# Kernel tuning notes

Measured on AMD Instinct MI355X. Metric: run time of the kernel, lower is better.

The kernel has to match this reference:

```python
import jax, jax.numpy as jnp
import numpy as np

HEADS = 16
DIM_HEAD = 64
DIM = 1024
LN_EPS = 1e-5


def _split_heads(x):
    # [b, n, h*d] -> [b, h, n, d]
    b, n, _ = x.shape
    return x.reshape(b, n, HEADS, DIM_HEAD).transpose(0, 2, 1, 3)


def _rmsnorm(x, gamma):
    # F.normalize over last dim, then * sqrt(dim_head) * gamma ([h,1,d])
    nrm = jnp.sqrt(jnp.sum(x * x, axis=-1, keepdims=True))
    normed = x / jnp.maximum(nrm, 1e-12)
    return normed * (DIM_HEAD ** 0.5) * gamma


def setup_inputs() -> dict:
    key = jax.random.key(0)
    ks = jax.random.split(key, 8)
    inner = HEADS * DIM_HEAD
    q = jax.random.normal(ks[0], (8, 128, DIM), dtype=jnp.float32)
    kv = jax.random.normal(ks[1], (8, 4096, DIM), dtype=jnp.float32)
    mask = jax.random.bernoulli(ks[2], 0.9, (8, 4096))  # bool, True = keep
    ln_w = jnp.ones((DIM,), dtype=jnp.float32)
    gamma_q = jnp.ones((HEADS, 1, DIM_HEAD), dtype=jnp.float32)
    gamma_k = jnp.ones((HEADS, 1, DIM_HEAD), dtype=jnp.float32)
    s = 1.0 / np.sqrt(DIM)
    Wq = jax.random.normal(ks[3], (DIM, inner), dtype=jnp.float32) * s
    Wkv = jax.random.normal(ks[4], (DIM, 2 * inner), dtype=jnp.float32) * s
    Wout = jax.random.normal(ks[5], (inner, DIM), dtype=jnp.float32) * (1.0 / np.sqrt(inner))
    return {"q": q, "kv": kv, "mask": mask, "ln_w": ln_w,
            "gamma_q": gamma_q, "gamma_k": gamma_k,
            "Wq": Wq, "Wkv": Wkv, "Wout": Wout}


def reference(q, kv, mask, ln_w, gamma_q, gamma_k, Wq, Wkv, Wout):
    # LayerNorm (no bias) on queries only
    mu = jnp.mean(q, axis=-1, keepdims=True)
    var = jnp.mean(jnp.square(q - mu), axis=-1, keepdims=True)
    qn = (q - mu) / jnp.sqrt(var + LN_EPS) * ln_w

    inner = HEADS * DIM_HEAD
    Q = qn @ Wq                      # [b, nq, inner]
    KVp = kv @ Wkv                   # [b, nkv, 2*inner]
    K, V = KVp[..., :inner], KVp[..., inner:]

    Qh = _rmsnorm(_split_heads(Q), gamma_q)   # [b, h, nq, d]
    Kh = _rmsnorm(_split_heads(K), gamma_k)   # [b, h, nkv, d]
    Vh = _split_heads(V)                      # [b, h, nkv, d]

    dots = jnp.einsum('bhnd,bhmd->bhnm', Qh, Kh)  # no 1/sqrt(d): scale lives in RMSNorm
    neg = -jnp.finfo(dots.dtype).max
    dots = jnp.where(mask[:, None, None, :], dots, neg)
    attn = jax.nn.softmax(dots, axis=-1)

    out = jnp.einsum('bhnm,bhmd->bhnd', attn, Vh)
    b, h, n, d = out.shape
    out = out.transpose(0, 2, 1, 3).reshape(b, n, h * d)
    return out @ Wout
```

## Files before the change

### kernel.cpp

```cpp
#include <hip/hip_runtime.h>
#include <cfloat>
#include <cstdint>


typedef _Float16 f16;
typedef _Float16 f16x8 __attribute__((ext_vector_type(8)));
typedef _Float16 f16x4 __attribute__((ext_vector_type(4)));
typedef float    f32x4 __attribute__((ext_vector_type(4)));

#define DEV __device__ __forceinline__

DEV f32x4 mfma16(f16x8 a, f16x8 b, f32x4 c) {
  return __builtin_amdgcn_mfma_f32_16x16x32_f16(a, b, c, 0, 0, 0);
}

DEV void gl_lds16(const void* g, void* l) {
  __builtin_amdgcn_global_load_lds(
      (const __attribute__((address_space(1))) uint32_t*)g,
      (__attribute__((address_space(3))) uint32_t*)l, 16, 0, 0);
}


__global__ __launch_bounds__(256) void cast_f16_kernel(
    const float* __restrict__ src, f16* __restrict__ dst, int n4) {
  int stride = gridDim.x * 256;
  for (int i = blockIdx.x * 256 + threadIdx.x; i < n4; i += stride) {
    float4 v = ((const float4*)src)[i];
    f16x4 o = { (f16)v.x, (f16)v.y, (f16)v.z, (f16)v.w };
    ((f16x4*)dst)[i] = o;
  }
}

__global__ __launch_bounds__(256) void transpose_cast_kernel(
    const float* __restrict__ src, f16* __restrict__ dst, int ldsrc, int lddst) {
  __shared__ float tile[32][33];
  int c0 = blockIdx.x * 32, r0 = blockIdx.y * 32;
  int tx = threadIdx.x & 31, ty = threadIdx.x >> 5;
  #pragma unroll
  for (int i = 0; i < 4; ++i)
    tile[ty + i * 8][tx] = src[(long)(r0 + ty + i * 8) * ldsrc + c0 + tx];
  __syncthreads();
  #pragma unroll
  for (int i = 0; i < 4; ++i)
    dst[(long)(c0 + ty + i * 8) * lddst + r0 + tx] = (f16)tile[tx][ty + i * 8];
}

__global__ __launch_bounds__(256) void ln_kernel(
    const float* __restrict__ q, const float* __restrict__ w, f16* __restrict__ qn) {
  int row = blockIdx.x, tid = threadIdx.x;
  float4 v = ((const float4*)(q + (long)row * 1024))[tid];
  float s1 = v.x + v.y + v.z + v.w;
  float s2 = v.x * v.x + v.y * v.y + v.z * v.z + v.w * v.w;
  #pragma unroll
  for (int off = 1; off < 64; off <<= 1) {
    s1 += __shfl_xor(s1, off);
    s2 += __shfl_xor(s2, off);
  }
  __shared__ float r1[4], r2[4];
  int wid = tid >> 6;
  if ((tid & 63) == 0) { r1[wid] = s1; r2[wid] = s2; }
  __syncthreads();
  s1 = r1[0] + r1[1] + r1[2] + r1[3];
  s2 = r2[0] + r2[1] + r2[2] + r2[3];
  float mu = s1 * (1.0f / 1024.0f);
  float var = s2 * (1.0f / 1024.0f) - mu * mu;
  float rstd = rsqrtf(var + 1e-5f);
  float4 wv = ((const float4*)w)[tid];
  f16x4 o = { (f16)((v.x - mu) * rstd * wv.x), (f16)((v.y - mu) * rstd * wv.y),
              (f16)((v.z - mu) * rstd * wv.z), (f16)((v.w - mu) * rstd * wv.w) };
  ((f16x4*)(qn + (long)row * 1024))[tid] = o;
}

template <int OUT_F16, int NORM>
__global__ __launch_bounds__(256) void gemm128(
    const f16* __restrict__ A, const f16* __restrict__ BT, void* __restrict__ C,
    const float* __restrict__ gamma,
    int M, int N, int K, int lda, int ldb, int ldc) {
  __shared__ f16 tA[128 * 32];
  __shared__ f16 tB[128 * 32];
  const int tid = threadIdx.x, lane = tid & 63, wid = tid >> 6;
  const int wr = wid >> 1, wc = wid & 1;
  const int c = lane & 15, g = lane >> 4;
  const int m0 = blockIdx.y * 128, n0 = blockIdx.x * 128;
  f32x4 acc[4][4] = {};
  for (int k0 = 0; k0 < K; k0 += 32) {
    __syncthreads();
    #pragma unroll
    for (int ii = 0; ii < 2; ++ii) {
      int i = tid + ii * 256;
      gl_lds16(A + (long)(m0 + (i >> 2)) * lda + k0 + (i & 3) * 8, tA + i * 8);
    }
    #pragma unroll
    for (int ii = 0; ii < 2; ++ii) {
      int i = tid + ii * 256;
      gl_lds16(BT + (long)(n0 + (i >> 2)) * ldb + k0 + (i & 3) * 8, tB + i * 8);
    }
    __syncthreads();
    f16x8 af[4], bfr[4];
    #pragma unroll
    for (int mi = 0; mi < 4; ++mi)
      af[mi] = *(const f16x8*)&tA[(wr * 64 + mi * 16 + c) * 32 + g * 8];
    #pragma unroll
    for (int ni = 0; ni < 4; ++ni)
      bfr[ni] = *(const f16x8*)&tB[(wc * 64 + ni * 16 + c) * 32 + g * 8];
    #pragma unroll
    for (int mi = 0; mi < 4; ++mi)
      #pragma unroll
      for (int ni = 0; ni < 4; ++ni)
        acc[mi][ni] = mfma16(af[mi], bfr[ni], acc[mi][ni]);
  }
  float gam[4];
  if (NORM) {
    #pragma unroll
    for (int ni = 0; ni < 4; ++ni) gam[ni] = gamma[n0 + wc * 64 + ni * 16 + c];
    #pragma unroll
    for (int mi = 0; mi < 4; ++mi)
      #pragma unroll
      for (int j = 0; j < 4; ++j) {
        float s = 0.f;
        #pragma unroll
        for (int ni = 0; ni < 4; ++ni) { float x = acc[mi][ni][j]; s += x * x; }
        s += __shfl_xor(s, 1); s += __shfl_xor(s, 2);
        s += __shfl_xor(s, 4); s += __shfl_xor(s, 8);
        float sc = 8.0f / fmaxf(sqrtf(s), 1e-12f);
        #pragma unroll
        for (int ni = 0; ni < 4; ++ni) acc[mi][ni][j] *= sc * gam[ni];
      }
  }
  #pragma unroll
  for (int mi = 0; mi < 4; ++mi)
    #pragma unroll
    for (int ni = 0; ni < 4; ++ni)
      #pragma unroll
      for (int j = 0; j < 4; ++j) {
        int row = m0 + wr * 64 + mi * 16 + g * 4 + j;
        int col = n0 + wc * 64 + ni * 16 + c;
        if (OUT_F16) ((f16*)C)[(long)row * ldc + col] = (f16)acc[mi][ni][j];
        else        ((float*)C)[(long)row * ldc + col] = acc[mi][ni][j];
      }
}

__global__ __launch_bounds__(512, 2) void gemm256(
    const f16* __restrict__ A, const f16* __restrict__ BT, f16* __restrict__ C,
    const float* __restrict__ gamma, int normLim,
    int K, int lda, int ldb, int ldc, int mtiles, int ntiles) {
  __shared__ f16 lds[4 * 16384];
  const int tid = threadIdx.x, lane = tid & 63, wid = tid >> 6;
  const int wr = wid >> 2, wc = wid & 3;
  const int c = lane & 15, g = lane >> 4;
  const int nwg = mtiles * ntiles, cpx = nwg >> 3;
  const int bid = blockIdx.x;
  const int wg = (bid & 7) * cpx + (bid >> 3);
  const int n0 = (wg % ntiles) * 256;
  const long m0 = (long)(wg / ntiles) * 256;

  const int nkt = K >> 5;
  const int r1 = tid >> 2, r2 = 128 + (tid >> 2), sl = tid & 3;
  const int sw1 = (sl ^ ((r1 >> 1) & 3)) << 3, sw2 = (sl ^ ((r2 >> 1) & 3)) << 3;

  f32x4 acc[8][4] = {};

  #define STAGE_A(kt_) do { int kt__ = (kt_);                                   \
    f16* dst = lds + ((kt__) & 3) * 16384; int k0 = (kt__) << 5;                \
    gl_lds16(A + (m0 + r1) * lda + k0 + sw1, dst + (long)tid * 8);              \
    gl_lds16(A + (m0 + r2) * lda + k0 + sw2, dst + (long)(tid + 512) * 8);      \
  } while (0)
  #define STAGE_B(kt_) do { int kt__ = (kt_);                                   \
    f16* dst = lds + ((kt__) & 3) * 16384 + 8192; int k0 = (kt__) << 5;         \
    gl_lds16(BT + (long)(n0 + r1) * ldb + k0 + sw1, dst + (long)tid * 8);       \
    gl_lds16(BT + (long)(n0 + r2) * ldb + k0 + sw2, dst + (long)(tid + 512) * 8);\
  } while (0)

  STAGE_A(0); STAGE_B(0); STAGE_A(1); STAGE_B(1);
  asm volatile("s_waitcnt vmcnt(4)" ::: "memory");
  __builtin_amdgcn_s_barrier();

  for (int kt = 0; kt < nkt; ++kt) {
    const f16* la = lds + (kt & 3) * 16384;
    const f16* lb = la + 8192;
    const bool pre = (kt + 2) < nkt;
    if (pre) STAGE_A(kt + 2);
    f16x8 bfr[4], afr[4];
    #pragma unroll
    for (int ni = 0; ni < 4; ++ni) {
      int r = wc * 64 + ni * 16 + c;
      bfr[ni] = *(const f16x8*)&lb[r * 32 + ((g ^ ((r >> 1) & 3)) << 3)];
    }
    #pragma unroll
    for (int q = 0; q < 4; ++q) {
      int r = wr * 128 + q * 16 + c;
      afr[q] = *(const f16x8*)&la[r * 32 + ((g ^ ((r >> 1) & 3)) << 3)];
    }
    __builtin_amdgcn_s_setprio(1);
    #pragma unroll
    for (int q = 0; q < 4; ++q)
      #pragma unroll
      for (int ni = 0; ni < 4; ++ni)
        acc[q][ni] = mfma16(afr[q], bfr[ni], acc[q][ni]);
    __builtin_amdgcn_s_setprio(0);
    if (pre) STAGE_B(kt + 2);
    #pragma unroll
    for (int q = 0; q < 4; ++q) {
      int r = wr * 128 + 64 + q * 16 + c;
      afr[q] = *(const f16x8*)&la[r * 32 + ((g ^ ((r >> 1) & 3)) << 3)];
    }
    __builtin_amdgcn_s_setprio(1);
    #pragma unroll
    for (int q = 0; q < 4; ++q)
      #pragma unroll
      for (int ni = 0; ni < 4; ++ni)
        acc[4 + q][ni] = mfma16(afr[q], bfr[ni], acc[4 + q][ni]);
    __builtin_amdgcn_s_setprio(0);
    if (pre) { asm volatile("s_waitcnt vmcnt(4)" ::: "memory"); }
    else     { asm volatile("s_waitcnt vmcnt(0)" ::: "memory"); }
    __builtin_amdgcn_s_barrier();
  }
  #undef STAGE_A
  #undef STAGE_B

  const int colbase = n0 + wc * 64;
  if (colbase < normLim) {
    float gam[4];
    #pragma unroll
    for (int ni = 0; ni < 4; ++ni) gam[ni] = gamma[colbase + ni * 16 + c];
    #pragma unroll
    for (int mi = 0; mi < 8; ++mi)
      #pragma unroll
      for (int j = 0; j < 4; ++j) {
        float s = 0.f;
        #pragma unroll
        for (int ni = 0; ni < 4; ++ni) { float x = acc[mi][ni][j]; s += x * x; }
        s += __shfl_xor(s, 1); s += __shfl_xor(s, 2);
        s += __shfl_xor(s, 4); s += __shfl_xor(s, 8);
        float sc = 8.0f / fmaxf(sqrtf(s), 1e-12f);
        #pragma unroll
        for (int ni = 0; ni < 4; ++ni) acc[mi][ni][j] *= sc * gam[ni];
      }
  }
  #pragma unroll
  for (int mi = 0; mi < 8; ++mi)
    #pragma unroll
    for (int j = 0; j < 4; ++j) {
      long row = m0 + wr * 128 + mi * 16 + g * 4 + j;
      #pragma unroll
      for (int ni = 0; ni < 4; ++ni)
        C[row * ldc + colbase + ni * 16 + c] = (f16)acc[mi][ni][j];
    }
}

__global__ __launch_bounds__(256) void attn_kernel(
    const f16* __restrict__ Q, const f16* __restrict__ KV,
    const int* __restrict__ mask, float* __restrict__ Opart,
    float* __restrict__ ml) {
  __shared__ f16 Kt[64 * 64];
  __shared__ f16 Vt[64 * 72];
  __shared__ f16 Pl[4 * 16 * 72];
  const int blk = blockIdx.x;
  const int chunk = blk >> 8, sub = blk & 255;
  const int half = sub & 1, h = (sub >> 1) & 15, b = sub >> 5;
  const int tid = threadIdx.x, lane = tid & 63, wid = tid >> 6;
  const int c = lane & 15, g = lane >> 4;

  const int qrow = b * 128 + half * 64 + wid * 16 + c;
  f16x8 qa[2];
  #pragma unroll
  for (int kk = 0; kk < 2; ++kk)
    qa[kk] = *(const f16x8*)&Q[(long)qrow * 1024 + h * 64 + kk * 32 + g * 8];

  float m_[4], l_[4];
  f32x4 o_[4];
  #pragma unroll
  for (int j = 0; j < 4; ++j) { m_[j] = -FLT_MAX; l_[j] = 0.f; }
  #pragma unroll
  for (int ni = 0; ni < 4; ++ni) o_[ni] = (f32x4){0.f, 0.f, 0.f, 0.f};

  const long kvbase = (long)b * 4096 * 2048;
  f16* Pw = Pl + wid * 16 * 72;

  for (int kt = chunk * 16; kt < chunk * 16 + 16; ++kt) {
    __syncthreads();
    #pragma unroll
    for (int ii = 0; ii < 2; ++ii) {
      int i = tid + ii * 256;
      int r = i >> 3, s = i & 7;
      gl_lds16(KV + kvbase + (long)(kt * 64 + r) * 2048 + h * 64 + ((s ^ (r & 7)) * 8),
               Kt + i * 8);
    }
    #pragma unroll
    for (int ii = 0; ii < 2; ++ii) {
      int i = tid + ii * 256;
      int kv = i & 63, d0 = (i >> 6) * 8;
      f16x8 v = *(const f16x8*)&KV[kvbase + (long)(kt * 64 + kv) * 2048 + 1024 + h * 64 + d0];
      #pragma unroll
      for (int j = 0; j < 8; ++j) Vt[(d0 + j) * 72 + kv] = v[j];
    }
    __syncthreads();

    f32x4 s4[4];
    #pragma unroll
    for (int ni = 0; ni < 4; ++ni) {
      s4[ni] = (f32x4){0.f, 0.f, 0.f, 0.f};
      int kvr = ni * 16 + c;
      #pragma unroll
      for (int kk = 0; kk < 2; ++kk) {
        int slot = (kk * 4 + g) ^ (kvr & 7);
        f16x8 kb = *(const f16x8*)&Kt[kvr * 64 + slot * 8];
        s4[ni] = mfma16(qa[kk], kb, s4[ni]);
      }
    }

    int msk[4];
    #pragma unroll
    for (int ni = 0; ni < 4; ++ni) {
      msk[ni] = mask[b * 4096 + kt * 64 + ni * 16 + c];
      if (!msk[ni]) s4[ni] = (f32x4){-FLT_MAX, -FLT_MAX, -FLT_MAX, -FLT_MAX};
    }

    float mnew[4], alpha[4], psum[4];
    #pragma unroll
    for (int j = 0; j < 4; ++j) {
      float v = fmaxf(fmaxf(s4[0][j], s4[1][j]), fmaxf(s4[2][j], s4[3][j]));
      v = fmaxf(v, __shfl_xor(v, 1));
      v = fmaxf(v, __shfl_xor(v, 2));
      v = fmaxf(v, __shfl_xor(v, 4));
      v = fmaxf(v, __shfl_xor(v, 8));
      mnew[j] = fmaxf(m_[j], v);
      alpha[j] = __expf(m_[j] - mnew[j]);
      m_[j] = mnew[j];
      psum[j] = 0.f;
    }
    f16 pb[4][4];
    #pragma unroll
    for (int ni = 0; ni < 4; ++ni)
      #pragma unroll
      for (int j = 0; j < 4; ++j) {
        float p = msk[ni] ? __expf(s4[ni][j] - mnew[j]) : 0.0f;
        psum[j] += p;
        pb[ni][j] = (f16)p;
      }
    #pragma unroll
    for (int j = 0; j < 4; ++j) {
      float ps = psum[j];
      ps += __shfl_xor(ps, 1);
      ps += __shfl_xor(ps, 2);
      ps += __shfl_xor(ps, 4);
      ps += __shfl_xor(ps, 8);
      l_[j] = alpha[j] * l_[j] + ps;
    }
    #pragma unroll
    for (int ni = 0; ni < 4; ++ni)
      #pragma unroll
      for (int j = 0; j < 4; ++j)
        Pw[(g * 4 + j) * 72 + ni * 16 + c] = pb[ni][j];
    #pragma unroll
    for (int ni = 0; ni < 4; ++ni)
      #pragma unroll
      for (int j = 0; j < 4; ++j)
        o_[ni][j] *= alpha[j];
    f16x8 pa[2];
    #pragma unroll
    for (int kk = 0; kk < 2; ++kk)
      pa[kk] = *(const f16x8*)&Pw[c * 72 + kk * 32 + g * 8];
    #pragma unroll
    for (int ni = 0; ni < 4; ++ni)
      #pragma unroll
      for (int kk = 0; kk < 2; ++kk) {
        f16x8 vb = *(const f16x8*)&Vt[(ni * 16 + c) * 72 + kk * 32 + g * 8];
        o_[ni] = mfma16(pa[kk], vb, o_[ni]);
      }
  }

  #pragma unroll
  for (int j = 0; j < 4; ++j) {
    int row = b * 128 + half * 64 + wid * 16 + g * 4 + j;
    #pragma unroll
    for (int ni = 0; ni < 4; ++ni)
      Opart[((long)chunk * 1024 + row) * 1024 + h * 64 + ni * 16 + c] = o_[ni][j];
    if (c == 0) {
      long u = (((long)chunk * 1024 + row) * 16 + h) * 2;
      ml[u] = m_[j];
      ml[u + 1] = l_[j];
    }
  }
}

__global__ __launch_bounds__(256) void attn_merge_kernel(
    const float* __restrict__ Opart, const float* __restrict__ ml,
    f16* __restrict__ Om) {
  int unit = blockIdx.x * 4 + (threadIdx.x >> 6);
  int lane = threadIdx.x & 63;
  int row = unit >> 4, h = unit & 15;
  float mc[4], lc[4], M = -FLT_MAX;
  #pragma unroll
  for (int cI = 0; cI < 4; ++cI) {
    long u = (((long)cI * 1024 + row) * 16 + h) * 2;
    mc[cI] = ml[u]; lc[cI] = ml[u + 1];
    M = fmaxf(M, mc[cI]);
  }
  float L = 0.f, o = 0.f;
  #pragma unroll
  for (int cI = 0; cI < 4; ++cI) {
    float w = __expf(mc[cI] - M);
    L += lc[cI] * w;
    o += Opart[((long)cI * 1024 + row) * 1024 + h * 64 + lane] * w;
  }
  Om[(long)row * 1024 + h * 64 + lane] = (f16)(o / fmaxf(L, 1e-30f));
}


extern "C" void kernel_launch(void* const* d_in, const int* in_sizes, int n_in,
                              void* d_out, int out_size, void* d_ws, size_t ws_size,
                              hipStream_t stream) {
  const float* q    = (const float*)d_in[0];
  const float* kv   = (const float*)d_in[1];
  const int*   mask = (const int*)d_in[2];
  const float* ln_w = (const float*)d_in[3];
  const float* gq   = (const float*)d_in[4];
  const float* gk   = (const float*)d_in[5];
  const float* Wq   = (const float*)d_in[6];
  const float* Wkv  = (const float*)d_in[7];
  const float* Wout = (const float*)d_in[8];
  float* out = (float*)d_out;
  char* ws = (char*)d_ws;
  const size_t MB = (size_t)1 << 20;
  f16* qn    = (f16*)(ws + 0 * MB);
  f16* Qm    = (f16*)(ws + 2 * MB);
  f16* Om    = (f16*)(ws + 4 * MB);
  f16* WqT   = (f16*)(ws + 6 * MB);
  f16* WkvT  = (f16*)(ws + 8 * MB);
  f16* WoutT = (f16*)(ws + 12 * MB);
  f16* kv16  = (f16*)(ws + 14 * MB);
  float* Opart = (float*)(ws + 14 * MB);
  float* mlb   = (float*)(ws + 30 * MB);
  f16* KVp   = (f16*)(ws + 78 * MB);

  cast_f16_kernel<<<2048, 256, 0, stream>>>(kv, kv16, 8 * 4096 * 1024 / 4);
  transpose_cast_kernel<<<dim3(32, 32), 256, 0, stream>>>(Wq, WqT, 1024, 1024);
  transpose_cast_kernel<<<dim3(64, 32), 256, 0, stream>>>(Wkv, WkvT, 2048, 1024);
  transpose_cast_kernel<<<dim3(32, 32), 256, 0, stream>>>(Wout, WoutT, 1024, 1024);
  ln_kernel<<<1024, 256, 0, stream>>>(q, ln_w, qn);
  gemm128<1, 1><<<dim3(8, 8), 256, 0, stream>>>(qn, WqT, Qm, gq,
                                                1024, 1024, 1024, 1024, 1024, 1024);
  gemm256<<<1024, 512, 0, stream>>>(kv16, WkvT, KVp, gk, 1024,
                                    1024, 1024, 1024, 2048, 128, 8);
  attn_kernel<<<1024, 256, 0, stream>>>(Qm, KVp, mask, Opart, mlb);
  attn_merge_kernel<<<4096, 256, 0, stream>>>(Opart, mlb, Om);
  gemm128<0, 0><<<dim3(8, 8), 256, 0, stream>>>(Om, WoutT, out, nullptr,
                                                1024, 1024, 1024, 1024, 1024, 1024);
}
```

Before: 515.5 us.

## Restructure KV GEMM into double-buffered 64-deep K pipeline and merge weight transposes

The 256x256 KV projection GEMM now stages 64-wide K slices into two LDS buffers. Its loop is unrolled into eight half-steps that interleave the next stage's global-to-LDS loads with MFMA blocks, and LDS fragment offsets are precomputed. The three weight transpose/cast launches are also merged into one kernel to cut launch overhead. The many extra barriers per iteration could add synchronization cost.

```diff
diff --git a/kernel.cpp b/kernel.cpp
--- a/kernel.cpp
+++ b/kernel.cpp
@@ -31,10 +31,19 @@
   }
 }
 
-__global__ __launch_bounds__(256) void transpose_cast_kernel(
-    const float* __restrict__ src, f16* __restrict__ dst, int ldsrc, int lddst) {
+__global__ __launch_bounds__(256) void transpose_all_kernel(
+    const float* __restrict__ Wq, const float* __restrict__ Wkv,
+    const float* __restrict__ Wout,
+    f16* __restrict__ WqT, f16* __restrict__ WkvT, f16* __restrict__ WoutT) {
   __shared__ float tile[32][33];
-  int c0 = blockIdx.x * 32, r0 = blockIdx.y * 32;
+  int b = blockIdx.x;
+  const float* src; f16* dst; int ldsrc, lddst, c0, r0;
+  if (b < 1024)      { src = Wq;   dst = WqT;   ldsrc = 1024; lddst = 1024;
+                       c0 = (b & 31) * 32;          r0 = (b >> 5) * 32; }
+  else if (b < 3072) { int bb = b - 1024; src = Wkv; dst = WkvT; ldsrc = 2048;
+                       lddst = 1024; c0 = (bb & 63) * 32; r0 = (bb >> 6) * 32; }
+  else               { int bb = b - 3072; src = Wout; dst = WoutT; ldsrc = 1024;
+                       lddst = 1024; c0 = (bb & 31) * 32; r0 = (bb >> 5) * 32; }
   int tx = threadIdx.x & 31, ty = threadIdx.x >> 5;
   #pragma unroll
   for (int i = 0; i < 4; ++i)
@@ -144,7 +153,7 @@
     const f16* __restrict__ A, const f16* __restrict__ BT, f16* __restrict__ C,
     const float* __restrict__ gamma, int normLim,
     int K, int lda, int ldb, int ldc, int mtiles, int ntiles) {
-  __shared__ f16 lds[4 * 16384];
+  __shared__ f16 lds[2 * 32768];
   const int tid = threadIdx.x, lane = tid & 63, wid = tid >> 6;
   const int wr = wid >> 2, wc = wid & 3;
   const int c = lane & 15, g = lane >> 4;
@@ -154,69 +163,95 @@
   const int n0 = (wg % ntiles) * 256;
   const long m0 = (long)(wg / ntiles) * 256;
 
-  const int nkt = K >> 5;
-  const int r1 = tid >> 2, r2 = 128 + (tid >> 2), sl = tid & 3;
-  const int sw1 = (sl ^ ((r1 >> 1) & 3)) << 3, sw2 = (sl ^ ((r2 >> 1) & 3)) << 3;
+  const int nkt = K >> 6;
+  const int row1 = tid >> 2, row2 = (tid >> 2) + 128, sl = tid & 3;
+  const int co1 = ((sl ^ ((row1 >> 1) & 3)) << 3);
+  const int co2 = ((sl ^ ((row2 >> 1) & 3)) << 3);
+
+  int aoff[8], boff[4];
+  #pragma unroll
+  for (int mi = 0; mi < 8; ++mi) {
+    int r = wr * 128 + mi * 16 + c;
+    aoff[mi] = r * 32 + ((g ^ ((r >> 1) & 3)) << 3);
+  }
+  #pragma unroll
+  for (int ni = 0; ni < 4; ++ni) {
+    int r = wc * 64 + ni * 16 + c;
+    boff[ni] = 16384 + r * 32 + ((g ^ ((r >> 1) & 3)) << 3);
+  }
 
   f32x4 acc[8][4] = {};
 
-  #define STAGE_A(kt_) do { int kt__ = (kt_);                                   \
-    f16* dst = lds + ((kt__) & 3) * 16384; int k0 = (kt__) << 5;                \
-    gl_lds16(A + (m0 + r1) * lda + k0 + sw1, dst + (long)tid * 8);              \
-    gl_lds16(A + (m0 + r2) * lda + k0 + sw2, dst + (long)(tid + 512) * 8);      \
+#define STAGE_A(kk_, t_) do {                                                   \
+    f16* dst = lds + ((t_) & 1) * 32768 + (kk_) * 8192;                          \
+    int k0 = ((t_) << 6) + (kk_) * 32;                                           \
+    gl_lds16(A + (m0 + row1) * lda + k0 + co1, dst + tid * 8);                   \
+    gl_lds16(A + (m0 + row2) * lda + k0 + co2, dst + (tid + 512) * 8);           \
   } while (0)
-  #define STAGE_B(kt_) do { int kt__ = (kt_);                                   \
-    f16* dst = lds + ((kt__) & 3) * 16384 + 8192; int k0 = (kt__) << 5;         \
-    gl_lds16(BT + (long)(n0 + r1) * ldb + k0 + sw1, dst + (long)tid * 8);       \
-    gl_lds16(BT + (long)(n0 + r2) * ldb + k0 + sw2, dst + (long)(tid + 512) * 8);\
+#define STAGE_B(kk_, t_) do {                                                   \
+    f16* dst = lds + ((t_) & 1) * 32768 + 16384 + (kk_) * 8192;                  \
+    int k0 = ((t_) << 6) + (kk_) * 32;                                           \
+    gl_lds16(BT + (long)(n0 + row1) * ldb + k0 + co1, dst + tid * 8);            \
+    gl_lds16(BT + (long)(n0 + row2) * ldb + k0 + co2, dst + (tid + 512) * 8);    \
   } while (0)
-
-  STAGE_A(0); STAGE_B(0); STAGE_A(1); STAGE_B(1);
-  asm volatile("s_waitcnt vmcnt(4)" ::: "memory");
-  __builtin_amdgcn_s_barrier();
-
-  for (int kt = 0; kt < nkt; ++kt) {
-    const f16* la = lds + (kt & 3) * 16384;
-    const f16* lb = la + 8192;
-    const bool pre = (kt + 2) < nkt;
-    if (pre) STAGE_A(kt + 2);
-    f16x8 bfr[4], afr[4];
-    #pragma unroll
-    for (int ni = 0; ni < 4; ++ni) {
-      int r = wc * 64 + ni * 16 + c;
-      bfr[ni] = *(const f16x8*)&lb[r * 32 + ((g ^ ((r >> 1) & 3)) << 3)];
-    }
-    #pragma unroll
-    for (int q = 0; q < 4; ++q) {
-      int r = wr * 128 + q * 16 + c;
-      afr[q] = *(const f16x8*)&la[r * 32 + ((g ^ ((r >> 1) & 3)) << 3)];
-    }
-    __builtin_amdgcn_s_setprio(1);
-    #pragma unroll
-    for (int q = 0; q < 4; ++q)
-      #pragma unroll
-      for (int ni = 0; ni < 4; ++ni)
-        acc[q][ni] = mfma16(afr[q], bfr[ni], acc[q][ni]);
+#define LD_A(kk_, mh_, buf_)                                                    \
+    _Pragma("unroll") for (int q = 0; q < 4; ++q)                               \
+      af[q] = *(const f16x8*)&lds[(buf_) + (kk_) * 8192 + aoff[(mh_) * 4 + q]];
+#define LD_B(kk_, buf_)                                                         \
+    _Pragma("unroll") for (int q = 0; q < 4; ++q)                               \
+      bf[q] = *(const f16x8*)&lds[(buf_) + (kk_) * 8192 + boff[q]];
+#define MM(mh_)                                                                 \
+    __builtin_amdgcn_s_setprio(1);                                              \
+    _Pragma("unroll") for (int q = 0; q < 4; ++q)                               \
+      _Pragma("unroll") for (int ni = 0; ni < 4; ++ni)                          \
+        acc[(mh_) * 4 + q][ni] = mfma16(af[q], bf[ni], acc[(mh_) * 4 + q][ni]); \
     __builtin_amdgcn_s_setprio(0);
-    if (pre) STAGE_B(kt + 2);
-    #pragma unroll
-    for (int q = 0; q < 4; ++q) {
-      int r = wr * 128 + 64 + q * 16 + c;
-      afr[q] = *(const f16x8*)&la[r * 32 + ((g ^ ((r >> 1) & 3)) << 3)];
-    }
-    __builtin_amdgcn_s_setprio(1);
-    #pragma unroll
-    for (int q = 0; q < 4; ++q)
-      #pragma unroll
-      for (int ni = 0; ni < 4; ++ni)
-        acc[4 + q][ni] = mfma16(afr[q], bfr[ni], acc[4 + q][ni]);
-    __builtin_amdgcn_s_setprio(0);
-    if (pre) { asm volatile("s_waitcnt vmcnt(4)" ::: "memory"); }
-    else     { asm volatile("s_waitcnt vmcnt(0)" ::: "memory"); }
-    __builtin_amdgcn_s_barrier();
-  }
-  #undef STAGE_A
-  #undef STAGE_B
+#define BAR __builtin_amdgcn_s_barrier()
+#define VM6 asm volatile("s_waitcnt vmcnt(6)" ::: "memory")
+#define VM0 asm volatile("s_waitcnt vmcnt(0)" ::: "memory")
+
+  STAGE_B(0, 0); STAGE_A(0, 0); STAGE_B(1, 0); STAGE_A(1, 0);
+  STAGE_B(0, 1); STAGE_A(0, 1); STAGE_B(1, 1);
+  VM6; BAR;
+
+  const int niter = nkt >> 1;
+  for (int it = 0; it < niter; ++it) {
+    const int t = it << 1;
+    const bool p2 = (t + 2) < nkt, p3 = (t + 3) < nkt;
+    f16x8 af[4], bf[4];
+    LD_B(0, 0); LD_A(0, 0, 0);
+    STAGE_A(1, t + 1);
+    BAR; MM(0); BAR;
+    LD_A(0, 1, 0);
+    if (p2) STAGE_B(0, t + 2);
+    BAR; MM(1); BAR;
+    LD_B(1, 0); LD_A(1, 0, 0);
+    if (p2) STAGE_A(0, t + 2);
+    BAR; MM(0); BAR;
+    LD_A(1, 1, 0);
+    if (p2) { STAGE_B(1, t + 2); VM6; } else { VM0; }
+    BAR; MM(1); BAR;
+    LD_B(0, 32768); LD_A(0, 0, 32768);
+    if (p2) STAGE_A(1, t + 2);
+    BAR; MM(0); BAR;
+    LD_A(0, 1, 32768);
+    if (p3) STAGE_B(0, t + 3);
+    BAR; MM(1); BAR;
+    LD_B(1, 32768); LD_A(1, 0, 32768);
+    if (p3) STAGE_A(0, t + 3);
+    BAR; MM(0); BAR;
+    LD_A(1, 1, 32768);
+    if (p3) { STAGE_B(1, t + 3); VM6; } else { VM0; }
+    BAR; MM(1); BAR;
+  }
+#undef STAGE_A
+#undef STAGE_B
+#undef LD_A
+#undef LD_B
+#undef MM
+#undef BAR
+#undef VM6
+#undef VM0
 
   const int colbase = n0 + wc * 64;
   if (colbase < normLim) {
@@ -435,9 +470,7 @@
   f16* KVp   = (f16*)(ws + 78 * MB);
 
   cast_f16_kernel<<<2048, 256, 0, stream>>>(kv, kv16, 8 * 4096 * 1024 / 4);
-  transpose_cast_kernel<<<dim3(32, 32), 256, 0, stream>>>(Wq, WqT, 1024, 1024);
-  transpose_cast_kernel<<<dim3(64, 32), 256, 0, stream>>>(Wkv, WkvT, 2048, 1024);
-  transpose_cast_kernel<<<dim3(32, 32), 256, 0, stream>>>(Wout, WoutT, 1024, 1024);
+  transpose_all_kernel<<<4096, 256, 0, stream>>>(Wq, Wkv, Wout, WqT, WkvT, WoutT);
   ln_kernel<<<1024, 256, 0, stream>>>(q, ln_w, qn);
   gemm128<1, 1><<<dim3(8, 8), 256, 0, stream>>>(qn, WqT, Qm, gq,
                                                 1024, 1024, 1024, 1024, 1024, 1024);
```

New measurement: 506.6 us. About the same (-1.7%).
